# Optimization experiments

Hardware: AMD Instinct MI355X
Metric: run time of the kernel (lower is better)

Reference implementation:

```python
import jax, jax.numpy as jnp
import numpy as np


def _cdist(a, b):
    # Euclidean distance between rows of a [M,D] and b [K,D] -> [M,K]
    a2 = jnp.sum(a * a, axis=-1)[:, None]
    b2 = jnp.sum(b * b, axis=-1)[None, :]
    d2 = a2 + b2 - 2.0 * (a @ b.T)
    return jnp.sqrt(jnp.maximum(d2, 1e-12))


def setup_inputs() -> dict:
    key = jax.random.key(0)
    k1, k2, k3 = jax.random.split(key, 3)
    L, N1, N2, P, D = 2, 8, 8, 1024, 768  # 2 output layers, 32x32 patches, ViT-B dim
    feats = jax.random.normal(k1, (L, N1, P, D), dtype=jnp.float32)
    nfeats = jax.random.normal(k2, (L, N2, P, D), dtype=jnp.float32)
    background_mask = jax.random.uniform(k3, (N1, P), dtype=jnp.float32)
    return {
        "feats": feats,
        "nfeats": nfeats,
        "background_mask": background_mask,
        "img_h": 512,
        "img_w": 512,
        "patch_size": 16,
    }


def reference(feats, nfeats, background_mask, img_h, img_w, patch_size):
    L, N1, P, D = feats.shape
    N2 = nfeats.shape[1]
    PH = img_h // patch_size
    PW = img_w // patch_size

    # L2-normalize patch features (as in Model.forward)
    f = feats / jnp.linalg.norm(feats, axis=-1, keepdims=True)
    nf = nfeats / jnp.linalg.norm(nfeats, axis=-1, keepdims=True)

    scores_list, pixel_list = [], []
    for l in range(L):  # small fixed number of output layers
        a = f[l].reshape(N1 * P, D)
        b = nf[l].reshape(N2 * P, D)
        # [N1,P,N2,P] -> [N1,N2,P,P], halved as in the original
        d = _cdist(a, b).reshape(N1, P, N2, P).transpose(0, 2, 1, 3) / 2.0
        sp = jnp.min(d, axis=-1)                       # [N1,N2,P] nearest normal patch
        sp = sp * background_mask[:, None, :]          # mask background patches
        sc = jnp.mean(jnp.max(sp, axis=-1), axis=-1)   # [N1] image score
        spatch = jnp.mean(sp, axis=1).reshape(N1, PH, PW)
        # bilinear, align_corners=False (half-pixel centers)
        spix = jax.image.resize(spatch, (N1, img_h, img_w), method="bilinear")
        scores_list.append(sc)
        pixel_list.append(spix)

    scores = jnp.mean(jnp.stack(scores_list, axis=0), axis=0)        # [N1]
    scores_pixel = jnp.mean(jnp.stack(pixel_list, axis=0), axis=0)   # [N1,H,W]
    return scores, scores_pixel
```

## Files before the change

kernel.cpp:

```cpp
#include <hip/hip_runtime.h>
#include <hip/hip_bf16.h>

using bf16 = __hip_bfloat16;
typedef __attribute__((ext_vector_type(8))) short short8;
typedef __attribute__((ext_vector_type(16))) float f32x16;

#define NLAY 2
#define NN1 8
#define NN2 8
#define PP 1024
#define DD 768
#define MROWS (NN1*PP)
#define BM 256
#define BN 256
#define BK 64
#define NKT (DD/BK)
#define NCT (MROWS/BN)

__global__ __launch_bounds__(256) void normalize_kernel(
    const float* __restrict__ in0, const float* __restrict__ in1,
    bf16* __restrict__ out0, bf16* __restrict__ out1) {
  int row  = blockIdx.x * 4 + (threadIdx.x >> 6);
  int lane = threadIdx.x & 63;
  const int half = NLAY * MROWS;
  const float* src;
  bf16* dst;
  if (row < half) { src = in0 + (size_t)row * DD;          dst = out0 + (size_t)row * DD; }
  else            { src = in1 + (size_t)(row - half) * DD; dst = out1 + (size_t)(row - half) * DD; }
  float4 v[3];
  float ss = 0.f;
#pragma unroll
  for (int i = 0; i < 3; i++) {
    v[i] = *reinterpret_cast<const float4*>(src + lane * 4 + i * 256);
    ss += v[i].x * v[i].x + v[i].y * v[i].y + v[i].z * v[i].z + v[i].w * v[i].w;
  }
#pragma unroll
  for (int off = 1; off < 64; off <<= 1) ss += __shfl_xor(ss, off);
  float rn = rsqrtf(ss);
#pragma unroll
  for (int i = 0; i < 3; i++) {
    bf16 tmp[4];
    tmp[0] = __float2bfloat16(v[i].x * rn);
    tmp[1] = __float2bfloat16(v[i].y * rn);
    tmp[2] = __float2bfloat16(v[i].z * rn);
    tmp[3] = __float2bfloat16(v[i].w * rn);
    *reinterpret_cast<uint2*>(dst + lane * 4 + i * 256) =
        *reinterpret_cast<const uint2*>(tmp);
  }
}


__device__ __forceinline__ short8 ld_frag(const bf16* h, int r, int slot) {
  return *reinterpret_cast<const short8*>(h + r * 64 + (((slot) ^ (r & 7)) << 3));
}

#define STAGE(Gbase, Lds) do {                                                  \
  _Pragma("unroll")                                                             \
  for (int i_ = 0; i_ < 2; i_++) {                                              \
    int u_ = i_ * 512 + t;                                                      \
    int r_ = u_ >> 3, s_ = u_ & 7;                                              \
    int sc_ = ((s_ ^ (r_ & 7)) << 3);                                           \
    __builtin_amdgcn_global_load_lds(                                           \
      (const __attribute__((address_space(1))) void*)((Gbase) + (size_t)r_ * DD + sc_), \
      (__attribute__((address_space(3))) void*)((Lds) + u_ * 8), 16, 0, 0);     \
  } } while (0)

#define VM2 asm volatile("s_waitcnt vmcnt(2)" ::: "memory")
#define VM0 asm volatile("s_waitcnt vmcnt(0)" ::: "memory")

#define LOAD_AF(buf, qm, kp)                                                    \
  _Pragma("unroll") for (int mt_ = 0; mt_ < 2; mt_++)                           \
  _Pragma("unroll") for (int j_ = 0; j_ < 2; j_++)                              \
    af_[mt_][j_] = ld_frag(&As[buf][qm][0], wr * 64 + mt_ * 32 + l31, ((kp) * 2 + j_) * 2 + hi);

#define LOAD_BF(buf, kp)                                                        \
  _Pragma("unroll") for (int n_ = 0; n_ < 2; n_++)                              \
  _Pragma("unroll") for (int j_ = 0; j_ < 2; j_++)                              \
    bf_[n_][j_] = ld_frag(&Bs[buf][hB][0], wcin * 64 + n_ * 32 + l31, ((kp) * 2 + j_) * 2 + hi);

#define MFMAS(qm)                                                               \
  __builtin_amdgcn_s_setprio(1);                                                \
  _Pragma("unroll") for (int j_ = 0; j_ < 2; j_++)                              \
  _Pragma("unroll") for (int mt_ = 0; mt_ < 2; mt_++)                           \
  _Pragma("unroll") for (int n_ = 0; n_ < 2; n_++)                              \
    acc[(qm) * 2 + mt_][n_] = __builtin_amdgcn_mfma_f32_32x32x16_bf16(          \
        af_[mt_][j_], bf_[n_][j_], acc[(qm) * 2 + mt_][n_], 0, 0, 0);           \
  __builtin_amdgcn_s_setprio(0);

#define PHASE_Q0(buf, kp, STG, VMC) do {                                        \
  LOAD_BF(buf, kp); LOAD_AF(buf, 0, kp);                                        \
  STG;                                                                          \
  __builtin_amdgcn_s_barrier();                                                 \
  asm volatile("s_waitcnt lgkmcnt(0)" ::: "memory");                            \
  MFMAS(0);                                                                     \
  VMC;                                                                          \
  __builtin_amdgcn_s_barrier();                                                 \
} while (0)

#define PHASE_Q1(buf, kp, STG, VMC) do {                                        \
  LOAD_AF(buf, 1, kp);                                                          \
  STG;                                                                          \
  __builtin_amdgcn_s_barrier();                                                 \
  asm volatile("s_waitcnt lgkmcnt(0)" ::: "memory");                            \
  MFMAS(1);                                                                     \
  VMC;                                                                          \
  __builtin_amdgcn_s_barrier();                                                 \
} while (0)

__global__ __launch_bounds__(512, 2) void gemm_max_kernel(
    const bf16* __restrict__ A, const bf16* __restrict__ Bm,
    float* __restrict__ partials) {
  __shared__ bf16 As[2][2][128 * 64];
  __shared__ bf16 Bs[2][2][128 * 64];
  __shared__ float red[4][256];

  const int id  = blockIdx.x;
  const int xcd = id & 7, p = id >> 3;
  const int l     = xcd >> 2;
  const int q     = p & 31, rnd = p >> 5;
  const int tiler = (xcd & 3) * 8 + (q & 7);
  const int tilec = rnd * 4 + (q >> 3);

  const bf16* Ab = A  + ((size_t)l * MROWS + (size_t)tiler * BM) * DD;
  const bf16* Bb = Bm + ((size_t)l * MROWS + (size_t)tilec * BN) * DD;

  const int t    = threadIdx.x;
  const int lane = t & 63;
  const int wave = t >> 6;
  const int wr   = wave >> 2;
  const int wc   = wave & 3;
  const int hB   = wc >> 1;
  const int wcin = wc & 1;
  const int l31  = lane & 31;
  const int hi   = lane >> 5;

  f32x16 acc[4][2];
#pragma unroll
  for (int a = 0; a < 4; a++)
#pragma unroll
    for (int n = 0; n < 2; n++)
#pragma unroll
      for (int j = 0; j < 16; j++) acc[a][n][j] = 0.f;

  STAGE(Ab,                      &As[0][0][0]);
  STAGE(Ab + (size_t)128 * DD,   &As[0][1][0]);
  STAGE(Bb,                      &Bs[0][0][0]);
  STAGE(Bb + (size_t)128 * DD,   &Bs[0][1][0]);
  STAGE(Ab + BK,                 &As[1][0][0]);
  VM2;
  __builtin_amdgcn_s_barrier();

  for (int i = 0; i < NKT / 2; i++) {
    const int O = 2 * i + 1, NE = 2 * i + 2, NO = 2 * i + 3;
    short8 af_[2][2], bf_[2][2];
    PHASE_Q0(0, 0, STAGE(Bb + (size_t)O * BK,                    &Bs[1][0][0]), (void)0);
    PHASE_Q1(0, 0, STAGE(Bb + (size_t)128 * DD + (size_t)O * BK, &Bs[1][1][0]), (void)0);
    PHASE_Q0(0, 1, STAGE(Ab + (size_t)128 * DD + (size_t)O * BK, &As[1][1][0]), (void)0);
    PHASE_Q1(0, 1, if (NE < NKT) STAGE(Ab + (size_t)NE * BK, &As[0][0][0]),
             if (NE < NKT) { VM2; } else { VM0; });
    PHASE_Q0(1, 0, if (NE < NKT) STAGE(Bb + (size_t)NE * BK, &Bs[0][0][0]), (void)0);
    PHASE_Q1(1, 0, if (NE < NKT) STAGE(Bb + (size_t)128 * DD + (size_t)NE * BK, &Bs[0][1][0]), (void)0);
    PHASE_Q0(1, 1, if (NE < NKT) STAGE(Ab + (size_t)128 * DD + (size_t)NE * BK, &As[0][1][0]), (void)0);
    PHASE_Q1(1, 1, if (NO < NKT) STAGE(Ab + (size_t)NO * BK, &As[1][0][0]), VM2);
  }

#pragma unroll
  for (int a = 0; a < 4; a++) {
#pragma unroll
    for (int j = 0; j < 16; j++) {
      float v = fmaxf(acc[a][0][j], acc[a][1][j]);
#pragma unroll
      for (int off = 1; off < 32; off <<= 1) v = fmaxf(v, __shfl_xor(v, off));
      if (l31 == 0) {
        int row = (a >> 1) * 128 + wr * 64 + (a & 1) * 32 + (j & 3) + 8 * (j >> 2) + 4 * hi;
        red[wc][row] = v;
      }
    }
  }
  __syncthreads();
  if (t < 256) {
    float v = fmaxf(fmaxf(red[0][t], red[1][t]), fmaxf(red[2][t], red[3][t]));
    partials[((size_t)l * MROWS + (size_t)tiler * BM + t) * NCT + tilec] = v;
  }
}

__global__ __launch_bounds__(1024) void reduce_kernel(
    const float* __restrict__ partials, const float* __restrict__ mask,
    float* __restrict__ scores, float* __restrict__ spatch) {
  const int n1 = blockIdx.x;
  const int p  = threadIdx.x;
  const int row = n1 * PP + p;
  const float mk = mask[row];

  float sp[16];
  float ssum = 0.f;
#pragma unroll
  for (int l = 0; l < NLAY; l++) {
    const float* pr = partials + ((size_t)l * MROWS + row) * NCT;
#pragma unroll
    for (int n2 = 0; n2 < NN2; n2++) {
      float md = pr[n2 * 4];
#pragma unroll
      for (int tt = 1; tt < 4; tt++) md = fmaxf(md, pr[n2 * 4 + tt]);
      float d2 = fmaxf(2.f - 2.f * md, 1e-12f);
      float s  = 0.5f * sqrtf(d2) * mk;
      sp[l * 8 + n2] = s;
      ssum += s;
    }
  }
  spatch[row] = ssum * (1.f / 16.f);

  __shared__ float wred[16][16];
  __shared__ float sres[16];
  const int lane = p & 63;
  const int wave = p >> 6;
#pragma unroll
  for (int v = 0; v < 16; v++) {
    float x = sp[v];
#pragma unroll
    for (int off = 1; off < 64; off <<= 1) x = fmaxf(x, __shfl_xor(x, off));
    if (lane == 0) wred[wave][v] = x;
  }
  __syncthreads();
  if (p < 16) {
    float x = wred[0][p];
#pragma unroll
    for (int w = 1; w < 16; w++) x = fmaxf(x, wred[w][p]);
    sres[p] = x;
  }
  __syncthreads();
  if (p == 0) {
    float s = 0.f;
#pragma unroll
    for (int v = 0; v < 16; v++) s += sres[v];
    scores[n1] = s * (1.f / 16.f);
  }
}

__global__ __launch_bounds__(256) void upsample_kernel(
    const float* __restrict__ spatch, float* __restrict__ out) {
  int idx = blockIdx.x * 256 + threadIdx.x;
  if (idx >= NN1 * 512 * 512) return;
  int x = idx & 511;
  int y = (idx >> 9) & 511;
  int n = idx >> 18;
  float sx = (x + 0.5f) * 0.0625f - 0.5f;
  float sy = (y + 0.5f) * 0.0625f - 0.5f;
  int x0 = (int)floorf(sx); float wx = sx - (float)x0;
  int y0 = (int)floorf(sy); float wy = sy - (float)y0;
  int x1 = min(x0 + 1, 31); x0 = max(x0, 0);
  int y1 = min(y0 + 1, 31); y0 = max(y0, 0);
  const float* s = spatch + n * PP;
  float v00 = s[y0 * 32 + x0], v01 = s[y0 * 32 + x1];
  float v10 = s[y1 * 32 + x0], v11 = s[y1 * 32 + x1];
  float v = (1.f - wy) * ((1.f - wx) * v00 + wx * v01) +
            wy * ((1.f - wx) * v10 + wx * v11);
  out[idx] = v;
}

extern "C" void kernel_launch(void* const* d_in, const int* in_sizes, int n_in,
                              void* d_out, int out_size, void* d_ws, size_t ws_size,
                              hipStream_t stream) {
  const float* feats  = (const float*)d_in[0];
  const float* nfeats = (const float*)d_in[1];
  const float* mask   = (const float*)d_in[2];
  float* out = (float*)d_out;

  bf16* Abf = (bf16*)d_ws;
  bf16* Bbf = Abf + (size_t)NLAY * MROWS * DD;
  float* partials = (float*)(Bbf + (size_t)NLAY * MROWS * DD);
  float* spatch   = partials + (size_t)NLAY * MROWS * NCT;

  normalize_kernel<<<(2 * NLAY * MROWS) / 4, 256, 0, stream>>>(feats, nfeats, Abf, Bbf);

  gemm_max_kernel<<<NCT * (MROWS / BM) * NLAY, 512, 0, stream>>>(Abf, Bbf, partials);

  reduce_kernel<<<NN1, 1024, 0, stream>>>(partials, mask, out, spatch);

  upsample_kernel<<<(NN1 * 512 * 512) / 256, 256, 0, stream>>>(spatch, out + 8);
}
```

Before: 438.4 us.

## Switch distance GEMM to 16x16x32 MFMA tiles with a four-phase k-loop

The bf16 GEMM inner loop now uses 16x16x32 MFMA instead of 32x32x16. Each wave covers a 64x64 output region split across both B halves, and each phase consumes a full 64-wide K slice. The k-tile schedule drops from eight phases to four, so there are fewer barrier pairs, and the global-to-LDS stages are regrouped per phase. The row-max epilogue is rewritten for the 16x16 accumulator layout. The trade-off is more accumulator vectors and fragment registers, plus a different LDS read pattern that could raise register pressure or bank conflicts.

```diff
diff --git a/kernel.cpp b/kernel.cpp
--- a/kernel.cpp
+++ b/kernel.cpp
@@ -3,7 +3,7 @@
 
 using bf16 = __hip_bfloat16;
 typedef __attribute__((ext_vector_type(8))) short short8;
-typedef __attribute__((ext_vector_type(16))) float f32x16;
+typedef __attribute__((ext_vector_type(4))) float f32x4;
 
 #define NLAY 2
 #define NN1 8
@@ -68,41 +68,31 @@
 #define VM2 asm volatile("s_waitcnt vmcnt(2)" ::: "memory")
 #define VM0 asm volatile("s_waitcnt vmcnt(0)" ::: "memory")
 
-#define LOAD_AF(buf, qm, kp)                                                    \
-  _Pragma("unroll") for (int mt_ = 0; mt_ < 2; mt_++)                           \
-  _Pragma("unroll") for (int j_ = 0; j_ < 2; j_++)                              \
-    af_[mt_][j_] = ld_frag(&As[buf][qm][0], wr * 64 + mt_ * 32 + l31, ((kp) * 2 + j_) * 2 + hi);
-
-#define LOAD_BF(buf, kp)                                                        \
+#define LOAD_A(buf, qm)                                                         \
+  _Pragma("unroll") for (int m_ = 0; m_ < 4; m_++)                              \
+  _Pragma("unroll") for (int ks_ = 0; ks_ < 2; ks_++)                           \
+    af_[m_][ks_] = ld_frag(&As[buf][qm][0], wr * 64 + m_ * 16 + rrow, ks_ * 4 + krow);
+
+#define LOAD_B(buf)                                                             \
+  _Pragma("unroll") for (int q_ = 0; q_ < 2; q_++)                              \
   _Pragma("unroll") for (int n_ = 0; n_ < 2; n_++)                              \
-  _Pragma("unroll") for (int j_ = 0; j_ < 2; j_++)                              \
-    bf_[n_][j_] = ld_frag(&Bs[buf][hB][0], wcin * 64 + n_ * 32 + l31, ((kp) * 2 + j_) * 2 + hi);
-
-#define MFMAS(qm)                                                               \
-  __builtin_amdgcn_s_setprio(1);                                                \
-  _Pragma("unroll") for (int j_ = 0; j_ < 2; j_++)                              \
-  _Pragma("unroll") for (int mt_ = 0; mt_ < 2; mt_++)                           \
-  _Pragma("unroll") for (int n_ = 0; n_ < 2; n_++)                              \
-    acc[(qm) * 2 + mt_][n_] = __builtin_amdgcn_mfma_f32_32x32x16_bf16(          \
-        af_[mt_][j_], bf_[n_][j_], acc[(qm) * 2 + mt_][n_], 0, 0, 0);           \
-  __builtin_amdgcn_s_setprio(0);
-
-#define PHASE_Q0(buf, kp, STG, VMC) do {                                        \
-  LOAD_BF(buf, kp); LOAD_AF(buf, 0, kp);                                        \
+  _Pragma("unroll") for (int ks_ = 0; ks_ < 2; ks_++)                           \
+    bf_[q_][n_][ks_] = ld_frag(&Bs[buf][q_][0], wc * 32 + n_ * 16 + rrow, ks_ * 4 + krow);
+
+#define PHASEQ(buf, qm, LDB, STG, VMC) do {                                     \
+  LOAD_A(buf, qm);                                                              \
+  LDB;                                                                          \
   STG;                                                                          \
   __builtin_amdgcn_s_barrier();                                                 \
   asm volatile("s_waitcnt lgkmcnt(0)" ::: "memory");                            \
-  MFMAS(0);                                                                     \
-  VMC;                                                                          \
-  __builtin_amdgcn_s_barrier();                                                 \
-} while (0)
-
-#define PHASE_Q1(buf, kp, STG, VMC) do {                                        \
-  LOAD_AF(buf, 1, kp);                                                          \
-  STG;                                                                          \
-  __builtin_amdgcn_s_barrier();                                                 \
-  asm volatile("s_waitcnt lgkmcnt(0)" ::: "memory");                            \
-  MFMAS(1);                                                                     \
+  __builtin_amdgcn_s_setprio(1);                                                \
+  _Pragma("unroll") for (int q_ = 0; q_ < 2; q_++)                              \
+  _Pragma("unroll") for (int n_ = 0; n_ < 2; n_++)                              \
+  _Pragma("unroll") for (int m_ = 0; m_ < 4; m_++)                              \
+  _Pragma("unroll") for (int ks_ = 0; ks_ < 2; ks_++)                           \
+    acc[(qm) * 4 + m_][q_ * 2 + n_] = __builtin_amdgcn_mfma_f32_16x16x32_bf16(  \
+        af_[m_][ks_], bf_[q_][n_][ks_], acc[(qm) * 4 + m_][q_ * 2 + n_], 0, 0, 0); \
+  __builtin_amdgcn_s_setprio(0);                                                \
   VMC;                                                                          \
   __builtin_amdgcn_s_barrier();                                                 \
 } while (0)
@@ -129,18 +119,14 @@
   const int wave = t >> 6;
   const int wr   = wave >> 2;
   const int wc   = wave & 3;
-  const int hB   = wc >> 1;
-  const int wcin = wc & 1;
-  const int l31  = lane & 31;
-  const int hi   = lane >> 5;
-
-  f32x16 acc[4][2];
-#pragma unroll
-  for (int a = 0; a < 4; a++)
-#pragma unroll
-    for (int n = 0; n < 2; n++)
-#pragma unroll
-      for (int j = 0; j < 16; j++) acc[a][n][j] = 0.f;
+  const int rrow = lane & 15;
+  const int krow = lane >> 4;
+
+  f32x4 acc[8][4];
+#pragma unroll
+  for (int m = 0; m < 8; m++)
+#pragma unroll
+    for (int n = 0; n < 4; n++) acc[m][n] = (f32x4){0.f, 0.f, 0.f, 0.f};
 
   STAGE(Ab,                      &As[0][0][0]);
   STAGE(Ab + (size_t)128 * DD,   &As[0][1][0]);
@@ -151,28 +137,36 @@
   __builtin_amdgcn_s_barrier();
 
   for (int i = 0; i < NKT / 2; i++) {
-    const int O = 2 * i + 1, NE = 2 * i + 2, NO = 2 * i + 3;
-    short8 af_[2][2], bf_[2][2];
-    PHASE_Q0(0, 0, STAGE(Bb + (size_t)O * BK,                    &Bs[1][0][0]), (void)0);
-    PHASE_Q1(0, 0, STAGE(Bb + (size_t)128 * DD + (size_t)O * BK, &Bs[1][1][0]), (void)0);
-    PHASE_Q0(0, 1, STAGE(Ab + (size_t)128 * DD + (size_t)O * BK, &As[1][1][0]), (void)0);
-    PHASE_Q1(0, 1, if (NE < NKT) STAGE(Ab + (size_t)NE * BK, &As[0][0][0]),
-             if (NE < NKT) { VM2; } else { VM0; });
-    PHASE_Q0(1, 0, if (NE < NKT) STAGE(Bb + (size_t)NE * BK, &Bs[0][0][0]), (void)0);
-    PHASE_Q1(1, 0, if (NE < NKT) STAGE(Bb + (size_t)128 * DD + (size_t)NE * BK, &Bs[0][1][0]), (void)0);
-    PHASE_Q0(1, 1, if (NE < NKT) STAGE(Ab + (size_t)128 * DD + (size_t)NE * BK, &As[0][1][0]), (void)0);
-    PHASE_Q1(1, 1, if (NO < NKT) STAGE(Ab + (size_t)NO * BK, &As[1][0][0]), VM2);
-  }
-
-#pragma unroll
-  for (int a = 0; a < 4; a++) {
-#pragma unroll
-    for (int j = 0; j < 16; j++) {
-      float v = fmaxf(acc[a][0][j], acc[a][1][j]);
-#pragma unroll
-      for (int off = 1; off < 32; off <<= 1) v = fmaxf(v, __shfl_xor(v, off));
-      if (l31 == 0) {
-        int row = (a >> 1) * 128 + wr * 64 + (a & 1) * 32 + (j & 3) + 8 * (j >> 2) + 4 * hi;
+    const int O = 2 * i + 1, E2 = 2 * i + 2, O2 = 2 * i + 3;
+    short8 af_[4][2], bf_[2][2][2];
+    PHASEQ(0, 0, LOAD_B(0),
+      { STAGE(Ab + (size_t)128 * DD + (size_t)O * BK, &As[1][1][0]);
+        STAGE(Bb + (size_t)O * BK,                    &Bs[1][0][0]);
+        STAGE(Bb + (size_t)128 * DD + (size_t)O * BK, &Bs[1][1][0]); }, (void)0);
+    PHASEQ(0, 1, (void)0,
+      if (E2 < NKT) STAGE(Ab + (size_t)E2 * BK, &As[0][0][0]),
+      if (E2 < NKT) { VM2; } else { VM0; });
+    PHASEQ(1, 0, LOAD_B(1),
+      if (E2 < NKT) { STAGE(Ab + (size_t)128 * DD + (size_t)E2 * BK, &As[0][1][0]);
+                      STAGE(Bb + (size_t)E2 * BK,                    &Bs[0][0][0]);
+                      STAGE(Bb + (size_t)128 * DD + (size_t)E2 * BK, &Bs[0][1][0]); }, (void)0);
+    PHASEQ(1, 1, (void)0,
+      if (O2 < NKT) STAGE(Ab + (size_t)O2 * BK, &As[1][0][0]),
+      if (O2 < NKT) { VM2; });
+  }
+
+#pragma unroll
+  for (int m = 0; m < 8; m++) {
+#pragma unroll
+    for (int j = 0; j < 4; j++) {
+      float v = acc[m][0][j];
+      v = fmaxf(v, acc[m][1][j]);
+      v = fmaxf(v, acc[m][2][j]);
+      v = fmaxf(v, acc[m][3][j]);
+#pragma unroll
+      for (int off = 1; off < 16; off <<= 1) v = fmaxf(v, __shfl_xor(v, off));
+      if (rrow == 0) {
+        int row = (m >> 2) * 128 + wr * 64 + (m & 3) * 16 + krow * 4 + j;
         red[wc][row] = v;
       }
     }
```

Result: faster. 360.3 us (-17.8%).
